# Performance work log

Hardware: AMD Instinct MI355X
Metric: run time of the kernel (lower is better)

Reference implementation:

```python
import jax, jax.numpy as jnp
import numpy as np

B, CIN, COUT, H, W = 8, 64, 64, 32, 64


def _conv3x3(x, w, b):
    # x: [B,Cin,H,W], w: [Cout,Cin,3,3], b: [Cout]; SAME padding (pad=1)
    y = jax.lax.conv_general_dilated(
        x, w, window_strides=(1, 1), padding=((1, 1), (1, 1)),
        dimension_numbers=('NCHW', 'OIHW', 'NCHW'))
    return y + b[None, :, None, None]


def setup_inputs() -> dict:
    key = jax.random.key(0)
    ks = jax.random.split(key, 7)
    fan_in = CIN * 3 * 3
    s = 1.0 / np.sqrt(fan_in)
    x = jax.random.normal(ks[0], (B, CIN, H, W), dtype=jnp.float32)
    wq = jax.random.uniform(ks[1], (COUT, CIN, 3, 3), jnp.float32, -s, s)
    bq = jax.random.uniform(ks[2], (COUT,), jnp.float32, -s, s)
    wk = jax.random.uniform(ks[3], (COUT, CIN, 3, 3), jnp.float32, -s, s)
    bk = jax.random.uniform(ks[4], (COUT,), jnp.float32, -s, s)
    wv = jax.random.uniform(ks[5], (COUT, CIN, 3, 3), jnp.float32, -s, s)
    bv = jax.random.uniform(ks[6], (COUT,), jnp.float32, -s, s)
    return {"x": x, "wq": wq, "bq": bq, "wk": wk, "bk": bk, "wv": wv, "bv": bv}


def reference(x, wq, bq, wk, bk, wv, bv):
    b, _, h, w = x.shape
    n = h * w
    q = _conv3x3(x, wq, bq).reshape(b, COUT, n)  # [B,C,N]
    k = _conv3x3(x, wk, bk).reshape(b, COUT, n)
    v = _conv3x3(x, wv, bv).reshape(b, COUT, n)
    # scores[b, i, j] = sum_c q[b,c,i] * k[b,c,j]  (NOTE: no 1/sqrt(d) scaling, as in source)
    scores = jnp.einsum('bci,bcj->bij', q, k)      # [B,N,N]
    attn = jax.nn.softmax(scores, axis=-1)
    out = jnp.einsum('bij,bcj->bci', attn, v)      # attn @ V^T, then transpose -> [B,C,N]
    return out.reshape(b, COUT, h, w)
```

## Files before the change

kernel.cpp:

```cpp
#include <hip/hip_runtime.h>
#include <hip/hip_bf16.h>

#define BATCH 8
#define NC    64
#define HH    32
#define WW    64
#define NN    2048
#define NCP   72
#define NCHUNK 4
#define KVBLK 64

typedef __attribute__((ext_vector_type(8))) short bf16x8;
typedef __attribute__((ext_vector_type(4))) short short4v;
typedef __attribute__((ext_vector_type(4))) float f32x4;

__device__ __forceinline__ unsigned short f2bf(float f) {
    union { float f; unsigned u; } v; v.f = f;
    unsigned r = v.u + 0x7fffu + ((v.u >> 16) & 1u);
    return (unsigned short)(r >> 16);
}
__device__ __forceinline__ float bf2f(unsigned short h) {
    union { unsigned u; float f; } v; v.u = ((unsigned)h) << 16;
    return v.f;
}

__device__ __forceinline__ bf16x8 load8(const unsigned short* a, const unsigned short* b) {
    short4v lo = *(const short4v*)a;
    short4v hi = *(const short4v*)b;
    return __builtin_shufflevector(lo, hi, 0, 1, 2, 3, 4, 5, 6, 7);
}

__device__ __forceinline__ int ci_of_slot(int j) {
    return (j & 32) | (((j >> 2) & 1) << 4) | (((j >> 3) & 3) << 2) | (j & 3);
}

__global__ __launch_bounds__(256) void prep_wx(
    const float* __restrict__ wq, const float* __restrict__ wk,
    const float* __restrict__ wv, const float* __restrict__ x,
    unsigned short* __restrict__ wb, unsigned short* __restrict__ xb)
{
    __shared__ unsigned short T[32][72];
    const int bid = blockIdx.x;
    const int tid = threadIdx.x;

    if (bid < 432) {
        const int idx = bid * 256 + tid;
        if (idx >= 9 * 192 * 64) return;
        const int j    = idx & 63;
        const int row  = (idx >> 6) % 192;
        const int tap  = idx / (192 * 64);
        const int ci   = ci_of_slot(j);
        const int conv = row >> 6;
        const int cout = row & 63;
        const float* ww = (conv == 0) ? wq : (conv == 1) ? wk : wv;
        wb[idx] = f2bf(ww[((size_t)cout * 64 + ci) * 9 + tap]);
        return;
    }

    const int bid2 = bid - 432;
    const int bi   = bid2 >> 6;
    const int rem  = bid2 & 63;
    const int y    = rem >> 1;
    const int x0   = (rem & 1) * 32;

#pragma unroll
    for (int pass = 0; pass < 8; ++pass) {
        const int idx = pass * 256 + tid;
        const int ci = idx >> 5, xx0 = idx & 31;
        T[xx0][ci] = f2bf(x[(((size_t)bi * 64 + ci) * 32 + y) * 64 + x0 + xx0]);
    }
    __syncthreads();

    {
        const int xx0 = tid >> 3, j8 = tid & 7;
        unsigned short h[8];
#pragma unroll
        for (int e = 0; e < 8; ++e)
            h[e] = T[xx0][ci_of_slot(j8 * 8 + e)];
        uint4 u;
        u.x = (unsigned)h[0] | ((unsigned)h[1] << 16);
        u.y = (unsigned)h[2] | ((unsigned)h[3] << 16);
        u.z = (unsigned)h[4] | ((unsigned)h[5] << 16);
        u.w = (unsigned)h[6] | ((unsigned)h[7] << 16);
        *(uint4*)(xb + ((((size_t)bi * 32 + y) * 64 + x0 + xx0) * 64) + j8 * 8) = u;
    }
}

__global__ __launch_bounds__(256) void conv_mfma(
    const unsigned short* __restrict__ xb,
    const unsigned short* __restrict__ wb,
    const float* __restrict__ bq, const float* __restrict__ bk,
    const float* __restrict__ bv,
    unsigned short* __restrict__ qT,
    unsigned short* __restrict__ kT,
    unsigned short* __restrict__ vv)
{
    __shared__ __align__(16) unsigned short Xs[3][34][NCP];
    __shared__ __align__(16) unsigned short Ws[2][96][NCP];

    const int bid = blockIdx.x;
    const int bi  = bid >> 7;
    const int rem = bid & 127;
    const int y   = rem >> 2;
    const int xh  = (rem >> 1) & 1;
    const int h   = rem & 1;
    const int tid = threadIdx.x;
    const int l   = tid & 63;
    const int w   = tid >> 6;
    const int g   = l >> 4;
    const int li  = l & 15;
    const int mq  = w & 1;
    const int pp  = w >> 1;
    const int x0  = xh * 32;

#pragma unroll
    for (int pass = 0; pass < 4; ++pass) {
        const int chunk = pass * 256 + tid;
        if (chunk < 816) {
            const int r  = chunk / 272;
            const int cc = chunk % 272;
            const int c  = cc >> 3, ci8 = cc & 7;
            const int yy = y + r - 1;
            const int xx = x0 + c - 1;
            uint4 d = {0, 0, 0, 0};
            if (yy >= 0 && yy < HH && xx >= 0 && xx < WW)
                d = *(const uint4*)(xb + ((((size_t)bi * HH + yy) * WW + xx) * 64) + ci8 * 8);
            *(uint4*)&Xs[r][c][ci8 * 8] = d;
        }
    }
#pragma unroll
    for (int pass = 0; pass < 3; ++pass) {
        const int chunk = pass * 256 + tid;
        const int row = chunk >> 3, ci8 = chunk & 7;
        uint4 d = *(const uint4*)(wb + ((size_t)(h * 96 + row)) * 64 + ci8 * 8);
        *(uint4*)&Ws[0][row][ci8 * 8] = d;
    }
    __syncthreads();

    f32x4 acc[3];
#pragma unroll
    for (int ct = 0; ct < 3; ++ct) acc[ct] = (f32x4){0, 0, 0, 0};

#pragma unroll
    for (int tap = 0; tap < 9; ++tap) {
        const int ky = tap / 3, kx = tap % 3;
        const int cur = tap & 1;

        uint4 wd[3];
        if (tap < 8) {
#pragma unroll
            for (int pass = 0; pass < 3; ++pass) {
                const int chunk = pass * 256 + tid;
                const int row = chunk >> 3, ci8 = chunk & 7;
                wd[pass] = *(const uint4*)(wb + ((size_t)(tap + 1) * 192 + h * 96 + row) * 64 + ci8 * 8);
            }
        }

        const int c = pp * 16 + li + kx;
        const bf16x8 xf0 = *(const bf16x8*)&Xs[ky][c][g * 8];
        const bf16x8 xf1 = *(const bf16x8*)&Xs[ky][c][32 + g * 8];

#pragma unroll
        for (int ct = 0; ct < 3; ++ct) {
            const int row = mq * 48 + ct * 16 + li;
            const bf16x8 wf0 = *(const bf16x8*)&Ws[cur][row][g * 8];
            const bf16x8 wf1 = *(const bf16x8*)&Ws[cur][row][32 + g * 8];
            acc[ct] = __builtin_amdgcn_mfma_f32_16x16x32_bf16(wf0, xf0, acc[ct], 0, 0, 0);
            acc[ct] = __builtin_amdgcn_mfma_f32_16x16x32_bf16(wf1, xf1, acc[ct], 0, 0, 0);
        }

        if (tap < 8) {
#pragma unroll
            for (int pass = 0; pass < 3; ++pass) {
                const int chunk = pass * 256 + tid;
                const int row = chunk >> 3, ci8 = chunk & 7;
                *(uint4*)&Ws[cur ^ 1][row][ci8 * 8] = wd[pass];
            }
            __syncthreads();
        }
    }

    const int n = y * 64 + x0 + pp * 16 + li;
#pragma unroll
    for (int ct = 0; ct < 3; ++ct) {
        const int rowbase = h * 96 + mq * 48 + ct * 16 + 4 * g;
        const int conv  = rowbase >> 6;
        const int cout0 = rowbase & 63;
        const float* bias = (conv == 0) ? bq : (conv == 1) ? bk : bv;
        float v0 = acc[ct][0] + bias[cout0 + 0];
        float v1 = acc[ct][1] + bias[cout0 + 1];
        float v2 = acc[ct][2] + bias[cout0 + 2];
        float v3 = acc[ct][3] + bias[cout0 + 3];
        if (conv < 2) {
            uint2 pk;
            pk.x = (unsigned)f2bf(v0) | ((unsigned)f2bf(v1) << 16);
            pk.y = (unsigned)f2bf(v2) | ((unsigned)f2bf(v3) << 16);
            unsigned short* dst = ((conv == 0) ? qT : kT) +
                                  ((size_t)bi * NN + n) * NC + cout0;
            *(uint2*)dst = pk;
        } else {
            vv[((size_t)bi * NC + cout0 + 0) * NN + n] = f2bf(v0);
            vv[((size_t)bi * NC + cout0 + 1) * NN + n] = f2bf(v1);
            vv[((size_t)bi * NC + cout0 + 2) * NN + n] = f2bf(v2);
            vv[((size_t)bi * NC + cout0 + 3) * NN + n] = f2bf(v3);
        }
    }
}

__global__ __launch_bounds__(256) void attn_mfma_split(
    const unsigned short* __restrict__ qT,
    const unsigned short* __restrict__ kT,
    const unsigned short* __restrict__ vv,
    unsigned short* __restrict__ Po,
    float* __restrict__ Pm, float* __restrict__ Pl)
{
    __shared__ __align__(16) unsigned short Ks[2][KVBLK][72];
    __shared__ __align__(16) unsigned short Vs[2][64][72];

    const int bid  = blockIdx.x;
    const int g8   = bid & 7;
    const int s    = bid >> 3;
    const int qq   = s >> 5;
    const int it   = s & 31;
    const int G    = g8 + 8 * qq;
    const int bi   = G >> 2;
    const int chunk= G & 3;

    const int tid = threadIdx.x;
    const int l   = tid & 63;
    const int w   = tid >> 6;
    const int g   = l >> 4;
    const int li  = l & 15;
    const int i0  = it * 64;
    const int jbase = chunk * (NN / NCHUNK);
    const int NT  = (NN / NCHUNK) / KVBLK;

    const unsigned short* qb = qT + (size_t)bi * NN * NC;
    const unsigned short* kb = kT + (size_t)bi * NN * NC;
    const unsigned short* vb = vv + (size_t)bi * NC * NN;

    const int qrow = i0 + w * 16 + li;
    const bf16x8 qf0 = load8(qb + (size_t)qrow * NC + 4 * g,      qb + (size_t)qrow * NC + 16 + 4 * g);
    const bf16x8 qf1 = load8(qb + (size_t)qrow * NC + 32 + 4 * g, qb + (size_t)qrow * NC + 48 + 4 * g);

    uint4 kd[2], vd[2];
#pragma unroll
    for (int u = 0; u < 2; ++u) {
        const int chunkid = u * 256 + tid;
        const int r = chunkid >> 3, c8 = chunkid & 7;
        kd[u] = *(const uint4*)(kb + ((size_t)(jbase + r)) * NC + c8 * 8);
        vd[u] = *(const uint4*)(vb + (size_t)r * NN + jbase + c8 * 8);
        *(uint4*)&Ks[0][r][c8 * 8] = kd[u];
        *(uint4*)&Vs[0][r][c8 * 8] = vd[u];
    }
    __syncthreads();

    f32x4 o0 = {0,0,0,0}, o1 = {0,0,0,0}, o2 = {0,0,0,0}, o3 = {0,0,0,0};
    float m = -1e30f, lsum = 0.0f;

    for (int t = 0; t < NT; ++t) {
        const int cur = t & 1;
        if (t < NT - 1) {
            const int j0 = jbase + (t + 1) * KVBLK;
#pragma unroll
            for (int u = 0; u < 2; ++u) {
                const int chunkid = u * 256 + tid;
                const int r = chunkid >> 3, c8 = chunkid & 7;
                kd[u] = *(const uint4*)(kb + ((size_t)(j0 + r)) * NC + c8 * 8);
                vd[u] = *(const uint4*)(vb + (size_t)r * NN + j0 + c8 * 8);
            }
        }

        f32x4 d[4];
        __builtin_amdgcn_s_setprio(1);
#pragma unroll
        for (int jb = 0; jb < 4; ++jb) {
            const bf16x8 kfa = load8(&Ks[cur][jb * 16 + li][4 * g],      &Ks[cur][jb * 16 + li][16 + 4 * g]);
            const bf16x8 kfb = load8(&Ks[cur][jb * 16 + li][32 + 4 * g], &Ks[cur][jb * 16 + li][48 + 4 * g]);
            const f32x4 z = {0,0,0,0};
            d[jb] = __builtin_amdgcn_mfma_f32_16x16x32_bf16(kfa, qf0, z, 0, 0, 0);
            d[jb] = __builtin_amdgcn_mfma_f32_16x16x32_bf16(kfb, qf1, d[jb], 0, 0, 0);
        }
        __builtin_amdgcn_s_setprio(0);

        float p[16];
#pragma unroll
        for (int jb = 0; jb < 4; ++jb)
#pragma unroll
            for (int e = 0; e < 4; ++e) p[jb * 4 + e] = d[jb][e];

        float pmax = p[0];
#pragma unroll
        for (int e = 1; e < 16; ++e) pmax = fmaxf(pmax, p[e]);
        pmax = fmaxf(pmax, __shfl_xor(pmax, 16));
        pmax = fmaxf(pmax, __shfl_xor(pmax, 32));

        if (!__all(pmax <= m)) {
            const float mn = fmaxf(m, pmax);
            const float alpha = __expf(m - mn);
            m = mn;
#pragma unroll
            for (int r = 0; r < 4; ++r) {
                const float ar = __shfl(alpha, 4 * g + r, 16);
                o0[r] *= ar; o1[r] *= ar; o2[r] *= ar; o3[r] *= ar;
            }
            lsum *= alpha;
        }

        float ls = 0.0f;
#pragma unroll
        for (int e = 0; e < 16; ++e) {
            p[e] = __expf(p[e] - m);
            ls += p[e];
        }
        ls += __shfl_xor(ls, 16);
        ls += __shfl_xor(ls, 32);
        lsum += ls;

        bf16x8 pf0, pf1;
#pragma unroll
        for (int e = 0; e < 8; ++e) {
            pf0[e] = (short)f2bf(p[e]);
            pf1[e] = (short)f2bf(p[8 + e]);
        }

        __builtin_amdgcn_s_setprio(1);
        {
            const bf16x8 va0 = load8(&Vs[cur][li][4 * g],      &Vs[cur][li][16 + 4 * g]);
            const bf16x8 va1 = load8(&Vs[cur][li][32 + 4 * g], &Vs[cur][li][48 + 4 * g]);
            o0 = __builtin_amdgcn_mfma_f32_16x16x32_bf16(pf0, va0, o0, 0, 0, 0);
            o0 = __builtin_amdgcn_mfma_f32_16x16x32_bf16(pf1, va1, o0, 0, 0, 0);
            const bf16x8 vb0 = load8(&Vs[cur][16 + li][4 * g],      &Vs[cur][16 + li][16 + 4 * g]);
            const bf16x8 vb1 = load8(&Vs[cur][16 + li][32 + 4 * g], &Vs[cur][16 + li][48 + 4 * g]);
            o1 = __builtin_amdgcn_mfma_f32_16x16x32_bf16(pf0, vb0, o1, 0, 0, 0);
            o1 = __builtin_amdgcn_mfma_f32_16x16x32_bf16(pf1, vb1, o1, 0, 0, 0);
            const bf16x8 vc0 = load8(&Vs[cur][32 + li][4 * g],      &Vs[cur][32 + li][16 + 4 * g]);
            const bf16x8 vc1 = load8(&Vs[cur][32 + li][32 + 4 * g], &Vs[cur][32 + li][48 + 4 * g]);
            o2 = __builtin_amdgcn_mfma_f32_16x16x32_bf16(pf0, vc0, o2, 0, 0, 0);
            o2 = __builtin_amdgcn_mfma_f32_16x16x32_bf16(pf1, vc1, o2, 0, 0, 0);
            const bf16x8 vd0 = load8(&Vs[cur][48 + li][4 * g],      &Vs[cur][48 + li][16 + 4 * g]);
            const bf16x8 vd1 = load8(&Vs[cur][48 + li][32 + 4 * g], &Vs[cur][48 + li][48 + 4 * g]);
            o3 = __builtin_amdgcn_mfma_f32_16x16x32_bf16(pf0, vd0, o3, 0, 0, 0);
            o3 = __builtin_amdgcn_mfma_f32_16x16x32_bf16(pf1, vd1, o3, 0, 0, 0);
        }
        __builtin_amdgcn_s_setprio(0);

        if (t < NT - 1) {
#pragma unroll
            for (int u = 0; u < 2; ++u) {
                const int chunkid = u * 256 + tid;
                const int r = chunkid >> 3, c8 = chunkid & 7;
                *(uint4*)&Ks[cur ^ 1][r][c8 * 8] = kd[u];
                *(uint4*)&Vs[cur ^ 1][r][c8 * 8] = vd[u];
            }
        }
        __syncthreads();
    }

    unsigned short* pob = Po + (((size_t)chunk * BATCH + bi) * NN) * NC;
#pragma unroll
    for (int r = 0; r < 4; ++r) {
        const int row = i0 + w * 16 + 4 * g + r;
        uint2 pk;
        pk.x = (unsigned)f2bf(o0[r]) | ((unsigned)f2bf(o1[r]) << 16);
        pk.y = (unsigned)f2bf(o2[r]) | ((unsigned)f2bf(o3[r]) << 16);
        *(uint2*)(pob + (size_t)row * NC + 4 * li) = pk;
    }
    if (g == 0) {
        const size_t mi = ((size_t)chunk * BATCH + bi) * NN + i0 + w * 16 + li;
        Pm[mi] = m;
        Pl[mi] = lsum;
    }
}

__global__ __launch_bounds__(256) void attn_combine(
    const unsigned short* __restrict__ Po,
    const float* __restrict__ Pm, const float* __restrict__ Pl,
    float* __restrict__ out)
{
    __shared__ float wf[NCHUNK][16];
    __shared__ float Os[16][66];

    const int bi = blockIdx.x >> 7;
    const int it = blockIdx.x & 127;
    const int i0 = it * 16;
    const int tid = threadIdx.x;

    if (tid < 64) {
        const int ch = tid >> 4, il = tid & 15;
        wf[ch][il] = Pm[((size_t)ch * BATCH + bi) * NN + i0 + il];
    }
    __syncthreads();
    if (tid < 16) {
        float mv[NCHUNK];
        float ms = -1e30f;
#pragma unroll
        for (int ch = 0; ch < NCHUNK; ++ch) {
            mv[ch] = wf[ch][tid];
            ms = fmaxf(ms, mv[ch]);
        }
        float denom = 0.0f;
        float ev[NCHUNK];
#pragma unroll
        for (int ch = 0; ch < NCHUNK; ++ch) {
            ev[ch] = __expf(mv[ch] - ms);
            denom = fmaf(ev[ch], Pl[((size_t)ch * BATCH + bi) * NN + i0 + tid], denom);
        }
        const float inv = 1.0f / denom;
#pragma unroll
        for (int ch = 0; ch < NCHUNK; ++ch)
            wf[ch][tid] = ev[ch] * inv;
    }
    __syncthreads();

    {
        const int rg = tid >> 6, ss = tid & 63;
        const int c = (ss & 3) * 16 + (ss >> 2);
#pragma unroll
        for (int k = 0; k < 4; ++k) {
            const int i = rg * 4 + k;
            float acc = 0.0f;
#pragma unroll
            for (int ch = 0; ch < NCHUNK; ++ch) {
                const float pv = bf2f(Po[(((size_t)ch * BATCH + bi) * NN + i0 + i) * NC + ss]);
                acc = fmaf(wf[ch][i], pv, acc);
            }
            Os[i][c] = acc;
        }
    }
    __syncthreads();

    {
        const int c = tid & 63, rg = tid >> 6;
        float* ob = out + ((size_t)bi * NC + c) * NN + i0 + rg * 4;
        *(float4*)ob = make_float4(Os[rg * 4 + 0][c], Os[rg * 4 + 1][c],
                                   Os[rg * 4 + 2][c], Os[rg * 4 + 3][c]);
    }
}

extern "C" void kernel_launch(void* const* d_in, const int* in_sizes, int n_in,
                              void* d_out, int out_size, void* d_ws, size_t ws_size,
                              hipStream_t stream)
{
    const float* x  = (const float*)d_in[0];
    const float* wq = (const float*)d_in[1];
    const float* bq = (const float*)d_in[2];
    const float* wk = (const float*)d_in[3];
    const float* bk = (const float*)d_in[4];
    const float* wv = (const float*)d_in[5];
    const float* bv = (const float*)d_in[6];

    unsigned short* ws16 = (unsigned short*)d_ws;
    const size_t TEN = (size_t)BATCH * NN * NC;
    unsigned short* qT = ws16;
    unsigned short* kT = ws16 + TEN;
    unsigned short* vv = ws16 + 2 * TEN;
    unsigned short* xb = ws16 + 3 * TEN;
    unsigned short* wb = ws16 + 4 * TEN;
    unsigned short* Po = ws16 + 4 * TEN + 131072;
    float* Pm = (float*)(ws16 + 4 * TEN + 131072 + (size_t)NCHUNK * TEN);
    float* Pl = Pm + (size_t)NCHUNK * BATCH * NN;
    float* out = (float*)d_out;

    prep_wx<<<dim3(944), 256, 0, stream>>>(wq, wk, wv, x, wb, xb);
    conv_mfma<<<dim3(1024), 256, 0, stream>>>(xb, wb, bq, bk, bv, qT, kT, vv);
    attn_mfma_split<<<dim3(BATCH * 32 * NCHUNK), 256, 0, stream>>>(qT, kT, vv, Po, Pm, Pl);
    attn_combine<<<dim3(BATCH * 128), 256, 0, stream>>>(Po, Pm, Pl, out);
}
```

Before: 56.79 us.

## Repartition conv kernel: full-row blocks over 16-channel slices, preload all tap weights

The conv kernel now gives each block one full image row (64 pixels) and a 16-output-channel slice, across 12 slices of the fused QKV outputs. That triples the grid to 3072 blocks. All nine taps' weights for the slice are loaded into shared memory up front, which removes the per-tap double-buffered weight prefetch and its eight barriers. Each wave now issues only 2 MFMAs per tap instead of 6. The input row halo is reloaded by 12 blocks instead of 4, so global and LDS traffic per unit of compute goes up.

```diff
diff --git a/kernel.cpp b/kernel.cpp
--- a/kernel.cpp
+++ b/kernel.cpp
@@ -95,115 +95,81 @@
     unsigned short* __restrict__ kT,
     unsigned short* __restrict__ vv)
 {
-    __shared__ __align__(16) unsigned short Xs[3][34][NCP];
-    __shared__ __align__(16) unsigned short Ws[2][96][NCP];
+    __shared__ __align__(16) unsigned short Xs[3][66][NCP];
+    __shared__ __align__(16) unsigned short Ws[9][16][NCP];
 
     const int bid = blockIdx.x;
-    const int bi  = bid >> 7;
-    const int rem = bid & 127;
-    const int y   = rem >> 2;
-    const int xh  = (rem >> 1) & 1;
-    const int h   = rem & 1;
+    const int mh  = bid % 12;
+    const int t2  = bid / 12;
+    const int y   = t2 & 31;
+    const int bi  = t2 >> 5;
     const int tid = threadIdx.x;
     const int l   = tid & 63;
     const int w   = tid >> 6;
     const int g   = l >> 4;
     const int li  = l & 15;
-    const int mq  = w & 1;
-    const int pp  = w >> 1;
-    const int x0  = xh * 32;
-
-#pragma unroll
-    for (int pass = 0; pass < 4; ++pass) {
-        const int chunk = pass * 256 + tid;
-        if (chunk < 816) {
-            const int r  = chunk / 272;
-            const int cc = chunk % 272;
-            const int c  = cc >> 3, ci8 = cc & 7;
-            const int yy = y + r - 1;
-            const int xx = x0 + c - 1;
+
+#pragma unroll
+    for (int r = 0; r < 3; ++r) {
+        const int yy = y + r - 1;
+#pragma unroll
+        for (int pass = 0; pass < 3; ++pass) {
+            const int chunk = pass * 256 + tid;
+            if (chunk >= 528) break;
+            const int c = chunk >> 3, ci8 = chunk & 7;
             uint4 d = {0, 0, 0, 0};
+            const int xx = c - 1;
             if (yy >= 0 && yy < HH && xx >= 0 && xx < WW)
                 d = *(const uint4*)(xb + ((((size_t)bi * HH + yy) * WW + xx) * 64) + ci8 * 8);
             *(uint4*)&Xs[r][c][ci8 * 8] = d;
         }
     }
 #pragma unroll
-    for (int pass = 0; pass < 3; ++pass) {
+    for (int pass = 0; pass < 5; ++pass) {
         const int chunk = pass * 256 + tid;
-        const int row = chunk >> 3, ci8 = chunk & 7;
-        uint4 d = *(const uint4*)(wb + ((size_t)(h * 96 + row)) * 64 + ci8 * 8);
-        *(uint4*)&Ws[0][row][ci8 * 8] = d;
-    }
-    __syncthreads();
-
-    f32x4 acc[3];
-#pragma unroll
-    for (int ct = 0; ct < 3; ++ct) acc[ct] = (f32x4){0, 0, 0, 0};
+        if (chunk >= 1152) break;
+        const int tap = chunk >> 7;
+        const int rr  = (chunk >> 3) & 15;
+        const int ci8 = chunk & 7;
+        uint4 d = *(const uint4*)(wb + ((size_t)(tap * 192 + mh * 16 + rr)) * 64 + ci8 * 8);
+        *(uint4*)&Ws[tap][rr][ci8 * 8] = d;
+    }
+    __syncthreads();
+
+    f32x4 acc = {0, 0, 0, 0};
 
 #pragma unroll
     for (int tap = 0; tap < 9; ++tap) {
         const int ky = tap / 3, kx = tap % 3;
-        const int cur = tap & 1;
-
-        uint4 wd[3];
-        if (tap < 8) {
-#pragma unroll
-            for (int pass = 0; pass < 3; ++pass) {
-                const int chunk = pass * 256 + tid;
-                const int row = chunk >> 3, ci8 = chunk & 7;
-                wd[pass] = *(const uint4*)(wb + ((size_t)(tap + 1) * 192 + h * 96 + row) * 64 + ci8 * 8);
-            }
-        }
-
-        const int c = pp * 16 + li + kx;
+        const bf16x8 wf0 = *(const bf16x8*)&Ws[tap][li][g * 8];
+        const bf16x8 wf1 = *(const bf16x8*)&Ws[tap][li][32 + g * 8];
+        const int c = w * 16 + li + kx;
         const bf16x8 xf0 = *(const bf16x8*)&Xs[ky][c][g * 8];
         const bf16x8 xf1 = *(const bf16x8*)&Xs[ky][c][32 + g * 8];
-
-#pragma unroll
-        for (int ct = 0; ct < 3; ++ct) {
-            const int row = mq * 48 + ct * 16 + li;
-            const bf16x8 wf0 = *(const bf16x8*)&Ws[cur][row][g * 8];
-            const bf16x8 wf1 = *(const bf16x8*)&Ws[cur][row][32 + g * 8];
-            acc[ct] = __builtin_amdgcn_mfma_f32_16x16x32_bf16(wf0, xf0, acc[ct], 0, 0, 0);
-            acc[ct] = __builtin_amdgcn_mfma_f32_16x16x32_bf16(wf1, xf1, acc[ct], 0, 0, 0);
-        }
-
-        if (tap < 8) {
-#pragma unroll
-            for (int pass = 0; pass < 3; ++pass) {
-                const int chunk = pass * 256 + tid;
-                const int row = chunk >> 3, ci8 = chunk & 7;
-                *(uint4*)&Ws[cur ^ 1][row][ci8 * 8] = wd[pass];
-            }
-            __syncthreads();
-        }
-    }
-
-    const int n = y * 64 + x0 + pp * 16 + li;
-#pragma unroll
-    for (int ct = 0; ct < 3; ++ct) {
-        const int rowbase = h * 96 + mq * 48 + ct * 16 + 4 * g;
-        const int conv  = rowbase >> 6;
-        const int cout0 = rowbase & 63;
-        const float* bias = (conv == 0) ? bq : (conv == 1) ? bk : bv;
-        float v0 = acc[ct][0] + bias[cout0 + 0];
-        float v1 = acc[ct][1] + bias[cout0 + 1];
-        float v2 = acc[ct][2] + bias[cout0 + 2];
-        float v3 = acc[ct][3] + bias[cout0 + 3];
-        if (conv < 2) {
-            uint2 pk;
-            pk.x = (unsigned)f2bf(v0) | ((unsigned)f2bf(v1) << 16);
-            pk.y = (unsigned)f2bf(v2) | ((unsigned)f2bf(v3) << 16);
-            unsigned short* dst = ((conv == 0) ? qT : kT) +
-                                  ((size_t)bi * NN + n) * NC + cout0;
-            *(uint2*)dst = pk;
-        } else {
-            vv[((size_t)bi * NC + cout0 + 0) * NN + n] = f2bf(v0);
-            vv[((size_t)bi * NC + cout0 + 1) * NN + n] = f2bf(v1);
-            vv[((size_t)bi * NC + cout0 + 2) * NN + n] = f2bf(v2);
-            vv[((size_t)bi * NC + cout0 + 3) * NN + n] = f2bf(v3);
-        }
+        acc = __builtin_amdgcn_mfma_f32_16x16x32_bf16(wf0, xf0, acc, 0, 0, 0);
+        acc = __builtin_amdgcn_mfma_f32_16x16x32_bf16(wf1, xf1, acc, 0, 0, 0);
+    }
+
+    const int n     = y * 64 + w * 16 + li;
+    const int conv  = mh >> 2;
+    const int cout0 = (mh & 3) * 16 + 4 * g;
+    const float* bias = (conv == 0) ? bq : (conv == 1) ? bk : bv;
+    float v0 = acc[0] + bias[cout0 + 0];
+    float v1 = acc[1] + bias[cout0 + 1];
+    float v2 = acc[2] + bias[cout0 + 2];
+    float v3 = acc[3] + bias[cout0 + 3];
+    if (conv < 2) {
+        uint2 pk;
+        pk.x = (unsigned)f2bf(v0) | ((unsigned)f2bf(v1) << 16);
+        pk.y = (unsigned)f2bf(v2) | ((unsigned)f2bf(v3) << 16);
+        unsigned short* dst = ((conv == 0) ? qT : kT) +
+                              ((size_t)bi * NN + n) * NC + cout0;
+        *(uint2*)dst = pk;
+    } else {
+        vv[((size_t)bi * NC + cout0 + 0) * NN + n] = f2bf(v0);
+        vv[((size_t)bi * NC + cout0 + 1) * NN + n] = f2bf(v1);
+        vv[((size_t)bi * NC + cout0 + 2) * NN + n] = f2bf(v2);
+        vv[((size_t)bi * NC + cout0 + 3) * NN + n] = f2bf(v3);
     }
 }
 
@@ -463,7 +429,7 @@
     float* out = (float*)d_out;
 
     prep_wx<<<dim3(944), 256, 0, stream>>>(wq, wk, wv, x, wb, xb);
-    conv_mfma<<<dim3(1024), 256, 0, stream>>>(xb, wb, bq, bk, bv, qT, kT, vv);
+    conv_mfma<<<dim3(3072), 256, 0, stream>>>(xb, wb, bq, bk, bv, qT, kT, vv);
     attn_mfma_split<<<dim3(BATCH * 32 * NCHUNK), 256, 0, stream>>>(qT, kT, vv, Po, Pm, Pl);
     attn_combine<<<dim3(BATCH * 128), 256, 0, stream>>>(Po, Pm, Pl, out);
 }
```

Result: slower. 63.23 us (+11.3%).

## Fuse split-KV combine into attention kernel via last-block atomic counter

Applied to the files above, without the earlier changes.

Removes the separate attn_combine launch. Each split-KV attention block bumps a per-(batch, query tile) atomic counter after writing its partial results, and the last of the four chunk blocks to finish performs the softmax merge and writes the output, reusing its shared memory. The counter is zeroed in the prep kernel. This saves one kernel launch and the tail of a dependent small kernel, in exchange for threadfences, an atomic per block, and a combine step that runs serially in whichever block finishes last.

```diff
diff --git a/kernel.cpp b/kernel.cpp
--- a/kernel.cpp
+++ b/kernel.cpp
@@ -37,11 +37,14 @@
 __global__ __launch_bounds__(256) void prep_wx(
     const float* __restrict__ wq, const float* __restrict__ wk,
     const float* __restrict__ wv, const float* __restrict__ x,
-    unsigned short* __restrict__ wb, unsigned short* __restrict__ xb)
+    unsigned short* __restrict__ wb, unsigned short* __restrict__ xb,
+    int* __restrict__ cnt)
 {
     __shared__ unsigned short T[32][72];
     const int bid = blockIdx.x;
     const int tid = threadIdx.x;
+
+    if (bid == 0 && tid < BATCH * 32) cnt[tid] = 0;
 
     if (bid < 432) {
         const int idx = bid * 256 + tid;
@@ -207,15 +210,18 @@
     }
 }
 
-__global__ __launch_bounds__(256) void attn_mfma_split(
+__global__ __launch_bounds__(256) void attn_fused(
     const unsigned short* __restrict__ qT,
     const unsigned short* __restrict__ kT,
     const unsigned short* __restrict__ vv,
     unsigned short* __restrict__ Po,
-    float* __restrict__ Pm, float* __restrict__ Pl)
+    float* __restrict__ Pm, float* __restrict__ Pl,
+    int* __restrict__ cnt,
+    float* __restrict__ out)
 {
     __shared__ __align__(16) unsigned short Ks[2][KVBLK][72];
     __shared__ __align__(16) unsigned short Vs[2][64][72];
+    __shared__ int sdone;
 
     const int bid  = blockIdx.x;
     const int g8   = bid & 7;
@@ -371,32 +377,30 @@
         Pm[mi] = m;
         Pl[mi] = lsum;
     }
-}
-
-__global__ __launch_bounds__(256) void attn_combine(
-    const unsigned short* __restrict__ Po,
-    const float* __restrict__ Pm, const float* __restrict__ Pl,
-    float* __restrict__ out)
-{
-    __shared__ float wf[NCHUNK][16];
-    __shared__ float Os[16][66];
-
-    const int bi = blockIdx.x >> 7;
-    const int it = blockIdx.x & 127;
-    const int i0 = it * 16;
-    const int tid = threadIdx.x;
-
+
+    __threadfence();
+    if (tid == 0) {
+        const int old = atomicAdd(&cnt[bi * 32 + it], 1);
+        sdone = (old == NCHUNK - 1);
+    }
+    __syncthreads();
+    if (!sdone) return;
+    __threadfence();
+
+    float* Os = (float*)&Ks[0][0][0];
+    float* wf = (float*)&Vs[0][0][0];
+
+    {
+        const int ch = tid >> 6, i = tid & 63;
+        wf[ch * 64 + i] = Pm[((size_t)ch * BATCH + bi) * NN + i0 + i];
+    }
+    __syncthreads();
     if (tid < 64) {
-        const int ch = tid >> 4, il = tid & 15;
-        wf[ch][il] = Pm[((size_t)ch * BATCH + bi) * NN + i0 + il];
-    }
-    __syncthreads();
-    if (tid < 16) {
         float mv[NCHUNK];
         float ms = -1e30f;
 #pragma unroll
         for (int ch = 0; ch < NCHUNK; ++ch) {
-            mv[ch] = wf[ch][tid];
+            mv[ch] = wf[ch * 64 + tid];
             ms = fmaxf(ms, mv[ch]);
         }
         float denom = 0.0f;
@@ -409,7 +413,7 @@
         const float inv = 1.0f / denom;
 #pragma unroll
         for (int ch = 0; ch < NCHUNK; ++ch)
-            wf[ch][tid] = ev[ch] * inv;
+            wf[ch * 64 + tid] = ev[ch] * inv;
     }
     __syncthreads();
 
@@ -417,24 +421,28 @@
         const int rg = tid >> 6, ss = tid & 63;
         const int c = (ss & 3) * 16 + (ss >> 2);
 #pragma unroll
-        for (int k = 0; k < 4; ++k) {
-            const int i = rg * 4 + k;
+        for (int k = 0; k < 16; ++k) {
+            const int i = rg * 16 + k;
             float acc = 0.0f;
 #pragma unroll
             for (int ch = 0; ch < NCHUNK; ++ch) {
                 const float pv = bf2f(Po[(((size_t)ch * BATCH + bi) * NN + i0 + i) * NC + ss]);
-                acc = fmaf(wf[ch][i], pv, acc);
-            }
-            Os[i][c] = acc;
+                acc = fmaf(wf[ch * 64 + i], pv, acc);
+            }
+            Os[i * 66 + c] = acc;
         }
     }
     __syncthreads();
 
     {
         const int c = tid & 63, rg = tid >> 6;
-        float* ob = out + ((size_t)bi * NC + c) * NN + i0 + rg * 4;
-        *(float4*)ob = make_float4(Os[rg * 4 + 0][c], Os[rg * 4 + 1][c],
-                                   Os[rg * 4 + 2][c], Os[rg * 4 + 3][c]);
+        float* ob = out + ((size_t)bi * NC + c) * NN + i0 + rg * 16;
+        float tmp[16];
+#pragma unroll
+        for (int k = 0; k < 16; ++k) tmp[k] = Os[(rg * 16 + k) * 66 + c];
+#pragma unroll
+        for (int k = 0; k < 16; k += 4)
+            *(float4*)(ob + k) = make_float4(tmp[k], tmp[k+1], tmp[k+2], tmp[k+3]);
     }
 }
 
@@ -460,10 +468,10 @@
     unsigned short* Po = ws16 + 4 * TEN + 131072;
     float* Pm = (float*)(ws16 + 4 * TEN + 131072 + (size_t)NCHUNK * TEN);
     float* Pl = Pm + (size_t)NCHUNK * BATCH * NN;
+    int*   cnt = (int*)(Pl + (size_t)NCHUNK * BATCH * NN);
     float* out = (float*)d_out;
 
-    prep_wx<<<dim3(944), 256, 0, stream>>>(wq, wk, wv, x, wb, xb);
+    prep_wx<<<dim3(944), 256, 0, stream>>>(wq, wk, wv, x, wb, xb, cnt);
     conv_mfma<<<dim3(1024), 256, 0, stream>>>(xb, wb, bq, bk, bv, qT, kT, vv);
-    attn_mfma_split<<<dim3(BATCH * 32 * NCHUNK), 256, 0, stream>>>(qT, kT, vv, Po, Pm, Pl);
-    attn_combine<<<dim3(BATCH * 128), 256, 0, stream>>>(Po, Pm, Pl, out);
-}
+    attn_fused<<<dim3(BATCH * 32 * NCHUNK), 256, 0, stream>>>(qT, kT, vv, Po, Pm, Pl, cnt, out);
+}
```

Measured after the change: 203.8 us. 3.59x slower.
